# Optimization experiments

Measured on AMD Instinct MI355X. Metric: run time of the kernel, lower is better.

## Reference

```python
import jax, jax.numpy as jnp
import numpy as np

S, B, D, N, DH = 2048, 2, 1024, 16, 64  # seq, batch, d_model, n_head, d_head
LN_EPS = 1e-5


def setup_inputs() -> dict:
    key = jax.random.key(0)
    ks = jax.random.split(key, 8)
    h = jax.random.normal(ks[0], (S, B, D), dtype=jnp.float32)
    Wq = jax.random.normal(ks[1], (D, N * DH), dtype=jnp.float32) * 0.02
    Wkv = jax.random.normal(ks[2], (D, 2 * N * DH), dtype=jnp.float32) * 0.02
    Wo = jax.random.normal(ks[3], (N * DH, D), dtype=jnp.float32) * 0.02
    ln_gamma = jnp.ones((D,), dtype=jnp.float32)
    ln_beta = jnp.zeros((D,), dtype=jnp.float32)
    # persistent compressive-memory state from a previous segment
    memory = jax.random.normal(ks[4], (B, N, DH, DH), dtype=jnp.float32)
    # normalization is a sum of (elu(k)+1) over ~S positions -> strictly positive, O(S)
    mem_norm = jax.random.uniform(ks[5], (B, 1, N, DH), dtype=jnp.float32) * S + 1.0
    gate_beta = jnp.ones((1,), dtype=jnp.float32) * 0.01  # beta_eps
    return {"h": h, "Wq": Wq, "Wkv": Wkv, "Wo": Wo, "ln_gamma": ln_gamma,
            "ln_beta": ln_beta, "memory": memory, "mem_norm": mem_norm,
            "gate_beta": gate_beta}


def reference(h, Wq, Wkv, Wo, ln_gamma, ln_beta, memory, mem_norm, gate_beta):
    scale = 1.0 / np.sqrt(DH).astype(np.float32)
    # projections (pre_lnorm=False, mems=None -> c == h)
    q = (h @ Wq).reshape(S, B, N, DH)
    k, v = jnp.split(h @ Wkv, 2, axis=-1)
    k = k.reshape(S, B, N, DH)
    v = v.reshape(S, B, N, DH)
    # local quadratic attention
    score = jnp.einsum('ibnd,jbnd->ijbn', q, k) * scale  # [S,S,B,N]
    prob = jax.nn.softmax(score, axis=1)
    attn_vec = jnp.einsum('ijbn,jbnd->ibnd', prob, v).reshape(S, B, N * DH)
    # memory retrieval (NOTE: source swaps K/V in the _update_memory call;
    # it is done under no_grad -> stop_gradient here)
    cached_Q = jax.nn.elu(q.swapaxes(0, 1)) + 1.0          # [B,S,N,DH]
    num = jnp.einsum('bsnk,bnkv->bsnv', cached_Q, memory)   # [B,S,N,DH]
    den = jnp.einsum('bsnk,bvnk->bsnv', cached_Q, mem_norm)  # [B,S,N,1]
    content_A = jax.lax.stop_gradient(num / den)            # [B,S,N,DH]
    # gated injection
    g = jax.nn.sigmoid(gate_beta)                           # [1]
    inj = g * content_A.swapaxes(0, 1).reshape(S, B, N * DH) + (1.0 - g) * attn_vec
    attn_out = inj @ Wo
    # post layernorm residual
    y = h + attn_out
    mu = jnp.mean(y, axis=-1, keepdims=True)
    var = jnp.mean((y - mu) ** 2, axis=-1, keepdims=True)
    return (y - mu) / jnp.sqrt(var + LN_EPS) * ln_gamma + ln_beta
```

## Files before the change

### kernel.cpp

```cpp
#include <hip/hip_runtime.h>


typedef unsigned short ushort_t;
typedef unsigned int uint32;

typedef __bf16 bf16x8 __attribute__((ext_vector_type(8)));
typedef float f32x4 __attribute__((ext_vector_type(4)));
typedef float f32x16 __attribute__((ext_vector_type(16)));
typedef unsigned short u16x8 __attribute__((ext_vector_type(8)));
typedef unsigned short u16x4 __attribute__((ext_vector_type(4)));
typedef unsigned int u32x4 __attribute__((ext_vector_type(4)));

typedef const __attribute__((address_space(1))) void gvoid_t;
typedef __attribute__((address_space(3))) void lvoid_t;

#define S_LEN 2048
#define BATCH 2
#define NHEAD 16

__device__ __forceinline__ ushort_t f2bf(float x) {
  union { float f; unsigned u; } c; c.f = x;
  unsigned r = (c.u + 0x7FFFu + ((c.u >> 16) & 1u)) >> 16;
  return (ushort_t)r;
}
__device__ __forceinline__ float bf2f(ushort_t v) {
  union { unsigned u; float f; } c; c.u = ((unsigned)v) << 16;
  return c.f;
}

__global__ __launch_bounds__(256) void k_cvt_h(const float* __restrict__ src,
                                               ushort_t* __restrict__ dst, int n4) {
  int idx = blockIdx.x * 256 + threadIdx.x;
  if (idx >= n4) return;
  float4 v = ((const float4*)src)[idx];
  u16x4 o; o[0] = f2bf(v.x); o[1] = f2bf(v.y); o[2] = f2bf(v.z); o[3] = f2bf(v.w);
  ((u16x4*)dst)[idx] = o;
}

__global__ __launch_bounds__(256) void k_cvt_wT3(const float* __restrict__ Wq,
                                                 const float* __restrict__ Wkv,
                                                 const float* __restrict__ Wo,
                                                 ushort_t* __restrict__ wT,
                                                 ushort_t* __restrict__ woT) {
  const int z = blockIdx.z;
  const float* W;
  ushort_t* WT;
  int N;
  if (z == 0)      { W = Wq;  WT = wT;                          N = 1024; }
  else if (z == 1) { W = Wkv; WT = wT + (size_t)1024 * 1024;    N = 2048; }
  else             { W = Wo;  WT = woT;                         N = 1024; }
  const int K = 1024;
  if (blockIdx.x * 32 >= N) return;
  __shared__ float tile[32][33];
  const int n0 = blockIdx.x * 32, k0 = blockIdx.y * 32;
  const int tx = threadIdx.x & 31, ty = threadIdx.x >> 5;
#pragma unroll
  for (int r = 0; r < 32; r += 8)
    tile[ty + r][tx] = W[(size_t)(k0 + ty + r) * N + n0 + tx];
  __syncthreads();
#pragma unroll
  for (int r = 0; r < 32; r += 8)
    WT[(size_t)(n0 + ty + r) * K + k0 + tx] = f2bf(tile[tx][ty + r]);
}

template <int OUT_BF16>
__global__ __launch_bounds__(256) void k_gemm_bt(const ushort_t* __restrict__ A,
                                                 const ushort_t* __restrict__ B,
                                                 void* __restrict__ Cv, int M, int N, int K,
                                                 int nbx) {
  __shared__ __attribute__((aligned(16))) ushort_t As[128 * 64];
  __shared__ __attribute__((aligned(16))) ushort_t Bs[128 * 64];
  const int per = gridDim.x >> 3;
  const int fl = (blockIdx.x & 7) * per + (blockIdx.x >> 3);
  const int m0 = (fl / nbx) * 128, n0 = (fl % nbx) * 128;
  const int tid = threadIdx.x, w = tid >> 6, lane = tid & 63;
  const int wm = (w >> 1) * 64, wn = (w & 1) * 64;
  const int l15 = lane & 15, l4 = lane >> 4;
  const int sw = ((lane & 7) ^ (lane >> 3)) << 3;
  f32x4 acc[4][4];
#pragma unroll
  for (int i = 0; i < 4; ++i)
#pragma unroll
    for (int j = 0; j < 4; ++j)
#pragma unroll
      for (int r = 0; r < 4; ++r) acc[i][j][r] = 0.f;

  for (int k0 = 0; k0 < K; k0 += 64) {
    __syncthreads();
#pragma unroll
    for (int r = 0; r < 4; ++r) {
      int rowb = r * 32 + w * 8;
      const ushort_t* ga = A + (size_t)(m0 + rowb + (lane >> 3)) * K + k0 + sw;
      const ushort_t* gb = B + (size_t)(n0 + rowb + (lane >> 3)) * K + k0 + sw;
      __builtin_amdgcn_global_load_lds((gvoid_t*)ga, (lvoid_t*)(As + rowb * 64), 16, 0, 0);
      __builtin_amdgcn_global_load_lds((gvoid_t*)gb, (lvoid_t*)(Bs + rowb * 64), 16, 0, 0);
    }
    __syncthreads();
#pragma unroll
    for (int kk = 0; kk < 2; ++kk) {
      bf16x8 af[4], bfr[4];
#pragma unroll
      for (int i = 0; i < 4; ++i) {
        int row = wm + i * 16 + l15;
        af[i] = *(const bf16x8*)&As[row * 64 + (((kk * 4 + l4) ^ (row & 7)) << 3)];
      }
#pragma unroll
      for (int j = 0; j < 4; ++j) {
        int row = wn + j * 16 + l15;
        bfr[j] = *(const bf16x8*)&Bs[row * 64 + (((kk * 4 + l4) ^ (row & 7)) << 3)];
      }
#pragma unroll
      for (int i = 0; i < 4; ++i)
#pragma unroll
        for (int j = 0; j < 4; ++j)
          acc[i][j] = __builtin_amdgcn_mfma_f32_16x16x32_bf16(af[i], bfr[j], acc[i][j], 0, 0, 0);
    }
  }
#pragma unroll
  for (int i = 0; i < 4; ++i)
#pragma unroll
    for (int j = 0; j < 4; ++j)
#pragma unroll
      for (int r = 0; r < 4; ++r) {
        int row = m0 + wm + i * 16 + l4 * 4 + r;
        int col = n0 + wn + j * 16 + l15;
        if (OUT_BF16)
          ((ushort_t*)Cv)[(size_t)row * N + col] = f2bf(acc[i][j][r]);
        else
          ((float*)Cv)[(size_t)row * N + col] = acc[i][j][r];
      }
}

__global__ __launch_bounds__(256) void k_gemm64(const ushort_t* __restrict__ A,
                                                const ushort_t* __restrict__ B,
                                                float* __restrict__ C, int M, int N, int K,
                                                int nbx) {
  __shared__ __attribute__((aligned(16))) ushort_t As[64 * 32];
  __shared__ __attribute__((aligned(16))) ushort_t Bs[128 * 32];
  const int per = gridDim.x >> 3;
  const int fl = (blockIdx.x & 7) * per + (blockIdx.x >> 3);
  const int m0 = (fl / nbx) * 64, n0 = (fl % nbx) * 128;
  const int tid = threadIdx.x, w = tid >> 6, lane = tid & 63;
  const int wn = w * 32;
  const int l15 = lane & 15, l4 = lane >> 4;
  f32x4 acc[4][2];
#pragma unroll
  for (int i = 0; i < 4; ++i)
#pragma unroll
    for (int j = 0; j < 2; ++j)
#pragma unroll
      for (int r = 0; r < 4; ++r) acc[i][j][r] = 0.f;

  for (int k0 = 0; k0 < K; k0 += 32) {
    __syncthreads();
    {
      int c = w * 64 + lane;
      const ushort_t* ga = A + (size_t)(m0 + (c >> 2)) * K + k0 + (c & 3) * 8;
      __builtin_amdgcn_global_load_lds((gvoid_t*)ga, (lvoid_t*)(As + w * 512), 16, 0, 0);
#pragma unroll
      for (int r = 0; r < 2; ++r) {
        int c2 = r * 256 + w * 64 + lane;
        const ushort_t* gb = B + (size_t)(n0 + (c2 >> 2)) * K + k0 + (c2 & 3) * 8;
        __builtin_amdgcn_global_load_lds((gvoid_t*)gb, (lvoid_t*)(Bs + r * 2048 + w * 512), 16, 0, 0);
      }
    }
    __syncthreads();
    bf16x8 af[4], bfr[2];
#pragma unroll
    for (int i = 0; i < 4; ++i) af[i] = *(const bf16x8*)&As[(i * 16 + l15) * 32 + l4 * 8];
#pragma unroll
    for (int j = 0; j < 2; ++j) bfr[j] = *(const bf16x8*)&Bs[(wn + j * 16 + l15) * 32 + l4 * 8];
#pragma unroll
    for (int i = 0; i < 4; ++i)
#pragma unroll
      for (int j = 0; j < 2; ++j)
        acc[i][j] = __builtin_amdgcn_mfma_f32_16x16x32_bf16(af[i], bfr[j], acc[i][j], 0, 0, 0);
  }
#pragma unroll
  for (int i = 0; i < 4; ++i)
#pragma unroll
    for (int j = 0; j < 2; ++j)
#pragma unroll
      for (int r = 0; r < 4; ++r)
        C[(size_t)(m0 + i * 16 + l4 * 4 + r) * N + n0 + wn + j * 16 + l15] = acc[i][j][r];
}

__global__ __launch_bounds__(256) void k_vt(const ushort_t* __restrict__ qkv,
                                            ushort_t* __restrict__ vt) {
  __shared__ uint32 tile[64 * 65];
  const int jt = blockIdx.x, bn = blockIdx.y, b = bn & 1, n = bn >> 1;
  const int tid = threadIdx.x;
  const int j0 = jt * 64;
#pragma unroll
  for (int rr = 0; rr < 2; ++rr) {
    int lin = rr * 2048 + tid * 8;
    int j = lin >> 6, d0 = lin & 63;
    u16x8 v = *(const u16x8*)(qkv + (size_t)(j0 + j) * 6144 + b * 3072 + 2048 + n * 64 + d0);
#pragma unroll
    for (int e = 0; e < 8; ++e) tile[j * 65 + d0 + e] = v[e];
  }
  __syncthreads();
#pragma unroll
  for (int rr = 0; rr < 2; ++rr) {
    int lin = rr * 2048 + tid * 8;
    int d = lin >> 6, jj = lin & 63;
    u16x8 o;
#pragma unroll
    for (int e = 0; e < 8; ++e) o[e] = (ushort_t)tile[(jj + e) * 65 + d];
    *(u16x8*)(vt + ((size_t)bn * 64 + d) * 2048 + j0 + jj) = o;
  }
}

__global__ __launch_bounds__(256, 4) void k_attn(const ushort_t* __restrict__ qkv,
                                                 const ushort_t* __restrict__ vt,
                                                 ushort_t* o0, ushort_t* o1,
                                                 float* __restrict__ l0,
                                                 float* __restrict__ l1) {
  __shared__ __attribute__((aligned(16))) ushort_t Ks[2][4096];
  __shared__ __attribute__((aligned(16))) ushort_t VTs[2][4096];
  const int bn = blockIdx.y, b = bn & 1, n = bn >> 1, z = blockIdx.z;
  const int tid = threadIdx.x, w = tid >> 6, lane = tid & 63;
  const int l31 = lane & 31, h = lane >> 5;
  const int qrow = blockIdx.x * 128 + w * 32 + l31;
  const size_t qoff = (size_t)qrow * 6144 + b * 3072 + n * 64;
  const float CEXP = 0.18033688011113723f;
  bf16x8 qf[4];
#pragma unroll
  for (int ks = 0; ks < 4; ++ks) {
    u16x8 qv = *(const u16x8*)(qkv + qoff + ks * 16 + h * 8);
    union { u16x8 u; bf16x8 v; } cu;
#pragma unroll
    for (int e = 0; e < 8; ++e) cu.u[e] = f2bf(bf2f(qv[e]) * CEXP);
    qf[ks] = cu.v;
  }
  const int fA = (l31 & 7) ^ (l31 >> 3);
  const int fB = fA ^ 4;

  const int t0 = z * 16;
  const int sw0 = (((lane & 7) ^ (lane >> 3) ^ (w * 2)) & 7) << 3;
  const int sw1 = (((lane & 7) ^ (lane >> 3) ^ (w * 2 + 1)) & 7) << 3;
  const ushort_t* kp0 = qkv + (size_t)(t0 * 64 + w * 16 + (lane >> 3)) * 6144 + b * 3072 + n * 64 + 1024 + sw0;
  const ushort_t* kp1 = qkv + (size_t)(t0 * 64 + w * 16 + 8 + (lane >> 3)) * 6144 + b * 3072 + n * 64 + 1024 + sw1;
  const ushort_t* vp0 = vt + ((size_t)bn * 64 + w * 16 + (lane >> 3)) * 2048 + t0 * 64 + sw0;
  const ushort_t* vp1 = vt + ((size_t)bn * 64 + w * 16 + 8 + (lane >> 3)) * 2048 + t0 * 64 + sw1;
  const size_t KSTRIDE = (size_t)64 * 6144;

  __builtin_amdgcn_global_load_lds((gvoid_t*)kp0, (lvoid_t*)(Ks[0] + (w * 16) * 64), 16, 0, 0);
  __builtin_amdgcn_global_load_lds((gvoid_t*)kp1, (lvoid_t*)(Ks[0] + (w * 16 + 8) * 64), 16, 0, 0);
  __builtin_amdgcn_global_load_lds((gvoid_t*)vp0, (lvoid_t*)(VTs[0] + (w * 16) * 64), 16, 0, 0);
  __builtin_amdgcn_global_load_lds((gvoid_t*)vp1, (lvoid_t*)(VTs[0] + (w * 16 + 8) * 64), 16, 0, 0);
  kp0 += KSTRIDE; kp1 += KSTRIDE; vp0 += 64; vp1 += 64;
  __syncthreads();

  f32x16 oacc[2];
#pragma unroll
  for (int r = 0; r < 16; ++r) { oacc[0][r] = 0.f; oacc[1][r] = 0.f; }
  float lsum = 0.f;

  for (int t = 0; t < 16; ++t) {
    const ushort_t* Kb = Ks[t & 1];
    const ushort_t* Vb = VTs[t & 1];
    if (t < 15) {
      ushort_t* kw = Ks[(t + 1) & 1];
      ushort_t* vw = VTs[(t + 1) & 1];
      __builtin_amdgcn_global_load_lds((gvoid_t*)kp0, (lvoid_t*)(kw + (w * 16) * 64), 16, 0, 0);
      __builtin_amdgcn_global_load_lds((gvoid_t*)kp1, (lvoid_t*)(kw + (w * 16 + 8) * 64), 16, 0, 0);
      __builtin_amdgcn_global_load_lds((gvoid_t*)vp0, (lvoid_t*)(vw + (w * 16) * 64), 16, 0, 0);
      __builtin_amdgcn_global_load_lds((gvoid_t*)vp1, (lvoid_t*)(vw + (w * 16 + 8) * 64), 16, 0, 0);
      kp0 += KSTRIDE; kp1 += KSTRIDE; vp0 += 64; vp1 += 64;
    }
#pragma unroll
    for (int jb = 0; jb < 2; ++jb) {
      f32x16 sv;
#pragma unroll
      for (int r = 0; r < 16; ++r) sv[r] = 0.f;
      const int rb = (jb * 32 + l31) * 64;
      const int fj = jb ? fB : fA;
      __builtin_amdgcn_s_setprio(1);
#pragma unroll
      for (int ks = 0; ks < 4; ++ks) {
        bf16x8 kf = *(const bf16x8*)&Kb[rb + ((((ks << 1) | h) ^ fj) << 3)];
        sv = __builtin_amdgcn_mfma_f32_32x32x16_bf16(kf, qf[ks], sv, 0, 0, 0);
      }
      __builtin_amdgcn_s_setprio(0);
#pragma unroll
      for (int r = 0; r < 16; ++r) sv[r] = __builtin_amdgcn_exp2f(sv[r]);
#pragma unroll
      for (int ks2 = 0; ks2 < 2; ++ks2) {
        const int q0 = ks2 * 2;
        uint32 X0, X1, Y0, Y1;
        asm volatile("v_cvt_pk_bf16_f32 %0, %1, %2" : "=v"(X0) : "v"(sv[q0 * 4 + 0]), "v"(sv[q0 * 4 + 1]));
        asm volatile("v_cvt_pk_bf16_f32 %0, %1, %2" : "=v"(X1) : "v"(sv[q0 * 4 + 2]), "v"(sv[q0 * 4 + 3]));
        asm volatile("v_cvt_pk_bf16_f32 %0, %1, %2" : "=v"(Y0) : "v"(sv[(q0 + 1) * 4 + 0]), "v"(sv[(q0 + 1) * 4 + 1]));
        asm volatile("v_cvt_pk_bf16_f32 %0, %1, %2" : "=v"(Y1) : "v"(sv[(q0 + 1) * 4 + 2]), "v"(sv[(q0 + 1) * 4 + 3]));
        asm volatile("v_permlane32_swap_b32 %0, %1" : "+v"(X0), "+v"(Y0));
        asm volatile("v_permlane32_swap_b32 %0, %1" : "+v"(X1), "+v"(Y1));
        union { u32x4 u; bf16x8 v; } pf;
        pf.u[0] = X0; pf.u[1] = X1; pf.u[2] = Y0; pf.u[3] = Y1;
        const int c = ((jb * 2 + ks2) << 1) | h;
        bf16x8 vf0 = *(const bf16x8*)&Vb[l31 * 64 + ((c ^ fA) << 3)];
        bf16x8 vf1 = *(const bf16x8*)&Vb[(32 + l31) * 64 + ((c ^ fB) << 3)];
        __builtin_amdgcn_s_setprio(1);
        oacc[0] = __builtin_amdgcn_mfma_f32_32x32x16_bf16(vf0, pf.v, oacc[0], 0, 0, 0);
        oacc[1] = __builtin_amdgcn_mfma_f32_32x32x16_bf16(vf1, pf.v, oacc[1], 0, 0, 0);
        __builtin_amdgcn_s_setprio(0);
      }
      float ls[8];
#pragma unroll
      for (int r = 0; r < 8; ++r) ls[r] = sv[r] + sv[r + 8];
#pragma unroll
      for (int st = 4; st >= 1; st >>= 1)
#pragma unroll
        for (int r = 0; r < st; ++r) ls[r] += ls[r + st];
      lsum += ls[0];
    }
    if (t < 15) __syncthreads();
  }
  const float l_run = lsum + __shfl_xor(lsum, 32);

  ushort_t* op = (z == 0) ? (o0 + (size_t)qrow * 2048 + b * 1024 + n * 64)
                          : (o1 + (size_t)qrow * 6144 + b * 3072 + 2048 + n * 64);
#pragma unroll
  for (int db = 0; db < 2; ++db)
#pragma unroll
    for (int qq = 0; qq < 4; ++qq) {
      u16x4 st;
#pragma unroll
      for (int m = 0; m < 4; ++m) st[m] = f2bf(oacc[db][qq * 4 + m]);
      *(u16x4*)(op + db * 32 + qq * 8 + h * 4) = st;
    }
  if (h == 0) {
    float* lp = (z == 0) ? l0 : l1;
    lp[qrow * 32 + bn] = l_run;
  }
}

__global__ __launch_bounds__(256) void k_gate2(const ushort_t* __restrict__ qkv,
                                               const ushort_t* __restrict__ o0,
                                               const float* __restrict__ l0,
                                               const float* __restrict__ l1,
                                               const float* __restrict__ mem,
                                               const float* __restrict__ mnorm,
                                               const float* __restrict__ gbeta,
                                               ushort_t* __restrict__ inj) {
  const int bn = blockIdx.y, b = bn & 1, n = bn >> 1;
  const int tid = threadIdx.x, w = tid >> 6, lane = tid & 63;
  const int l31 = lane & 31, h = lane >> 5;
  const int qrow = blockIdx.x * 128 + w * 32 + l31;
  const size_t qoff = (size_t)qrow * 6144 + b * 3072 + n * 64;

  float den = 0.f;
  bf16x8 cqf[4];
  const float* nrm = mnorm + (size_t)(b * NHEAD + n) * 64;
#pragma unroll
  for (int ks = 0; ks < 4; ++ks) {
    u16x8 qv = *(const u16x8*)(qkv + qoff + ks * 16 + h * 8);
    union { u16x8 u; bf16x8 v; } cu;
#pragma unroll
    for (int e = 0; e < 8; ++e) {
      float x = bf2f(qv[e]);
      float c = (x > 0.f) ? (x + 1.f) : __builtin_amdgcn_exp2f(x * 1.4426950408889634f);
      cu.u[e] = f2bf(c);
      den += c * nrm[ks * 16 + h * 8 + e];
    }
    cqf[ks] = cu.v;
  }
  den += __shfl_xor(den, 32);

  const float* mb = mem + (size_t)(b * NHEAD + n) * 4096;
  f32x16 accv[2];
#pragma unroll
  for (int r = 0; r < 16; ++r) { accv[0][r] = 0.f; accv[1][r] = 0.f; }
#pragma unroll
  for (int db = 0; db < 2; ++db)
#pragma unroll
    for (int ks = 0; ks < 4; ++ks) {
      union { u16x8 u; bf16x8 v; } af;
#pragma unroll
      for (int e = 0; e < 8; ++e)
        af.u[e] = f2bf(mb[(size_t)(ks * 16 + h * 8 + e) * 64 + db * 32 + l31]);
      accv[db] = __builtin_amdgcn_mfma_f32_32x32x16_bf16(af.v, cqf[ks], accv[db], 0, 0, 0);
    }

  const float lsum = l0[qrow * 32 + bn] + l1[qrow * 32 + bn];
  float g = 1.f / (1.f + expf(-gbeta[0]));
  float rden = 1.f / den, invl = 1.f / lsum;
  const ushort_t* p0 = o0 + (size_t)qrow * 2048 + b * 1024 + n * 64;
  const ushort_t* p1 = qkv + (size_t)qrow * 6144 + b * 3072 + 2048 + n * 64;
  ushort_t* op = inj + (size_t)qrow * 2048 + b * 1024 + n * 64;
#pragma unroll
  for (int db = 0; db < 2; ++db)
#pragma unroll
    for (int qq = 0; qq < 4; ++qq) {
      const int off = db * 32 + qq * 8 + h * 4;
      u16x4 a0 = *(const u16x4*)(p0 + off);
      u16x4 a1 = *(const u16x4*)(p1 + off);
      u16x4 st;
#pragma unroll
      for (int m = 0; m < 4; ++m) {
        float av = (bf2f(a0[m]) + bf2f(a1[m])) * invl;
        float content = accv[db][qq * 4 + m] * rden;
        st[m] = f2bf(g * content + (1.f - g) * av);
      }
      *(u16x4*)(op + off) = st;
    }
}

__global__ __launch_bounds__(256) void k_ln(const float* __restrict__ h,
                                            const float* __restrict__ ao,
                                            const float* __restrict__ gam,
                                            const float* __restrict__ bet,
                                            float* __restrict__ out) {
  const int m = blockIdx.x, t = threadIdx.x;
  const int lane = t & 63, w = t >> 6;
  __shared__ float redS[4], redQ[4];
  const size_t base = (size_t)m * 1024;
  float4 hv = ((const float4*)(h + base))[t];
  float4 avv = ((const float4*)(ao + base))[t];
  float y0 = hv.x + avv.x, y1 = hv.y + avv.y, y2 = hv.z + avv.z, y3 = hv.w + avv.w;
  float s = y0 + y1 + y2 + y3;
  float sq = y0 * y0 + y1 * y1 + y2 * y2 + y3 * y3;
#pragma unroll
  for (int mk = 32; mk >= 1; mk >>= 1) { s += __shfl_xor(s, mk); sq += __shfl_xor(sq, mk); }
  if (lane == 0) { redS[w] = s; redQ[w] = sq; }
  __syncthreads();
  float Ssum = redS[0] + redS[1] + redS[2] + redS[3];
  float Qsum = redQ[0] + redQ[1] + redQ[2] + redQ[3];
  float mu = Ssum * (1.f / 1024.f);
  float var = Qsum * (1.f / 1024.f) - mu * mu;
  float rstd = rsqrtf(var + 1e-5f);
  float4 g = ((const float4*)gam)[t];
  float4 bt = ((const float4*)bet)[t];
  float4 o;
  o.x = (y0 - mu) * rstd * g.x + bt.x;
  o.y = (y1 - mu) * rstd * g.y + bt.y;
  o.z = (y2 - mu) * rstd * g.z + bt.z;
  o.w = (y3 - mu) * rstd * g.w + bt.w;
  ((float4*)(out + base))[t] = o;
}

extern "C" void kernel_launch(void* const* d_in, const int* in_sizes, int n_in,
                              void* d_out, int out_size, void* d_ws, size_t ws_size,
                              hipStream_t stream) {
  const float* h = (const float*)d_in[0];
  const float* Wq = (const float*)d_in[1];
  const float* Wkv = (const float*)d_in[2];
  const float* Wo = (const float*)d_in[3];
  const float* gam = (const float*)d_in[4];
  const float* bet = (const float*)d_in[5];
  const float* mem = (const float*)d_in[6];
  const float* mnorm = (const float*)d_in[7];
  const float* gbeta = (const float*)d_in[8];
  float* out = (float*)d_out;

  char* ws = (char*)d_ws;
  ushort_t* hb  = (ushort_t*)(ws);
  ushort_t* wT  = (ushort_t*)(ws + (size_t)(8u << 20));
  ushort_t* woT = (ushort_t*)(ws + (size_t)(14u << 20));
  ushort_t* qkv = (ushort_t*)(ws + (size_t)(16u << 20));
  float*    ao  = (float*)   (ws + (size_t)(16u << 20));
  ushort_t* vtb = (ushort_t*)(ws + (size_t)(40u << 20));
  ushort_t* o0  = hb;
  float*    l0  = (float*)(ws + (size_t)(8u << 20));
  float*    l1  = (float*)(ws + (size_t)(8u << 20) + (1u << 18));
  ushort_t* inj = vtb;

  k_cvt_h<<<4096, 256, 0, stream>>>(h, hb, 1048576);
  k_cvt_wT3<<<dim3(64, 32, 3), 256, 0, stream>>>(Wq, Wkv, Wo, wT, woT);
  k_gemm_bt<1><<<768, 256, 0, stream>>>(hb, wT, (void*)qkv, 4096, 3072, 1024, 24);
  k_vt<<<dim3(32, 32), 256, 0, stream>>>(qkv, vtb);
  k_attn<<<dim3(16, 32, 2), 256, 0, stream>>>(qkv, vtb, o0, qkv, l0, l1);
  k_gate2<<<dim3(16, 32), 256, 0, stream>>>(qkv, o0, l0, l1, mem, mnorm, gbeta, inj);
  k_gemm64<<<512, 256, 0, stream>>>(inj, woT, ao, 4096, 1024, 1024, 8);
  k_ln<<<4096, 256, 0, stream>>>(h, ao, gam, bet, out);
}
```

Measured before the change: 144.4 us.

## Merge conversion kernels and deepen output GEMM K-tile with swizzled LDS

The separate h-to-bf16 and weight-transpose kernels become one launch, with an extra z-slice that converts h. The output-projection GEMM now loads 64-wide K tiles instead of 32, halving loop iterations and barriers. It also uses an XOR swizzle on LDS addresses to avoid bank conflicts on the fragment reads. LDS use per block doubles, which may lower occupancy.

```diff
diff --git a/kernel.cpp b/kernel.cpp
--- a/kernel.cpp
+++ b/kernel.cpp
@@ -28,27 +28,31 @@
   return c.f;
 }
 
-__global__ __launch_bounds__(256) void k_cvt_h(const float* __restrict__ src,
-                                               ushort_t* __restrict__ dst, int n4) {
-  int idx = blockIdx.x * 256 + threadIdx.x;
-  if (idx >= n4) return;
-  float4 v = ((const float4*)src)[idx];
-  u16x4 o; o[0] = f2bf(v.x); o[1] = f2bf(v.y); o[2] = f2bf(v.z); o[3] = f2bf(v.w);
-  ((u16x4*)dst)[idx] = o;
-}
-
-__global__ __launch_bounds__(256) void k_cvt_wT3(const float* __restrict__ Wq,
+__global__ __launch_bounds__(256) void k_cvt_all(const float* __restrict__ h,
+                                                 const float* __restrict__ Wq,
                                                  const float* __restrict__ Wkv,
                                                  const float* __restrict__ Wo,
+                                                 ushort_t* __restrict__ hb,
                                                  ushort_t* __restrict__ wT,
                                                  ushort_t* __restrict__ woT) {
   const int z = blockIdx.z;
+  if (z == 3) {
+    int idx = (blockIdx.y * 64 + blockIdx.x) * 256 + threadIdx.x;
+#pragma unroll
+    for (int i = 0; i < 2; ++i) {
+      int e = idx + i * 524288;
+      float4 v = ((const float4*)h)[e];
+      u16x4 o; o[0] = f2bf(v.x); o[1] = f2bf(v.y); o[2] = f2bf(v.z); o[3] = f2bf(v.w);
+      ((u16x4*)hb)[e] = o;
+    }
+    return;
+  }
   const float* W;
   ushort_t* WT;
   int N;
-  if (z == 0)      { W = Wq;  WT = wT;                          N = 1024; }
-  else if (z == 1) { W = Wkv; WT = wT + (size_t)1024 * 1024;    N = 2048; }
-  else             { W = Wo;  WT = woT;                         N = 1024; }
+  if (z == 0)      { W = Wq;  WT = wT;                        N = 1024; }
+  else if (z == 1) { W = Wkv; WT = wT + (size_t)1024 * 1024;  N = 2048; }
+  else             { W = Wo;  WT = woT;                       N = 1024; }
   const int K = 1024;
   if (blockIdx.x * 32 >= N) return;
   __shared__ float tile[32][33];
@@ -135,14 +139,15 @@
                                                 const ushort_t* __restrict__ B,
                                                 float* __restrict__ C, int M, int N, int K,
                                                 int nbx) {
-  __shared__ __attribute__((aligned(16))) ushort_t As[64 * 32];
-  __shared__ __attribute__((aligned(16))) ushort_t Bs[128 * 32];
+  __shared__ __attribute__((aligned(16))) ushort_t As[64 * 64];
+  __shared__ __attribute__((aligned(16))) ushort_t Bs[128 * 64];
   const int per = gridDim.x >> 3;
   const int fl = (blockIdx.x & 7) * per + (blockIdx.x >> 3);
   const int m0 = (fl / nbx) * 64, n0 = (fl % nbx) * 128;
   const int tid = threadIdx.x, w = tid >> 6, lane = tid & 63;
   const int wn = w * 32;
   const int l15 = lane & 15, l4 = lane >> 4;
+  const int sw = ((lane & 7) ^ (lane >> 3)) << 3;
   f32x4 acc[4][2];
 #pragma unroll
   for (int i = 0; i < 4; ++i)
@@ -151,30 +156,40 @@
 #pragma unroll
       for (int r = 0; r < 4; ++r) acc[i][j][r] = 0.f;
 
-  for (int k0 = 0; k0 < K; k0 += 32) {
+  for (int k0 = 0; k0 < K; k0 += 64) {
     __syncthreads();
-    {
-      int c = w * 64 + lane;
-      const ushort_t* ga = A + (size_t)(m0 + (c >> 2)) * K + k0 + (c & 3) * 8;
-      __builtin_amdgcn_global_load_lds((gvoid_t*)ga, (lvoid_t*)(As + w * 512), 16, 0, 0);
-#pragma unroll
-      for (int r = 0; r < 2; ++r) {
-        int c2 = r * 256 + w * 64 + lane;
-        const ushort_t* gb = B + (size_t)(n0 + (c2 >> 2)) * K + k0 + (c2 & 3) * 8;
-        __builtin_amdgcn_global_load_lds((gvoid_t*)gb, (lvoid_t*)(Bs + r * 2048 + w * 512), 16, 0, 0);
-      }
+#pragma unroll
+    for (int r = 0; r < 2; ++r) {
+      int rowb = w * 16 + r * 8;
+      const ushort_t* ga = A + (size_t)(m0 + rowb + (lane >> 3)) * K + k0 + sw;
+      __builtin_amdgcn_global_load_lds((gvoid_t*)ga, (lvoid_t*)(As + rowb * 64), 16, 0, 0);
+    }
+#pragma unroll
+    for (int r = 0; r < 4; ++r) {
+      int rowb = w * 32 + r * 8;
+      const ushort_t* gb = B + (size_t)(n0 + rowb + (lane >> 3)) * K + k0 + sw;
+      __builtin_amdgcn_global_load_lds((gvoid_t*)gb, (lvoid_t*)(Bs + rowb * 64), 16, 0, 0);
     }
     __syncthreads();
-    bf16x8 af[4], bfr[2];
-#pragma unroll
-    for (int i = 0; i < 4; ++i) af[i] = *(const bf16x8*)&As[(i * 16 + l15) * 32 + l4 * 8];
-#pragma unroll
-    for (int j = 0; j < 2; ++j) bfr[j] = *(const bf16x8*)&Bs[(wn + j * 16 + l15) * 32 + l4 * 8];
-#pragma unroll
-    for (int i = 0; i < 4; ++i)
-#pragma unroll
-      for (int j = 0; j < 2; ++j)
-        acc[i][j] = __builtin_amdgcn_mfma_f32_16x16x32_bf16(af[i], bfr[j], acc[i][j], 0, 0, 0);
+#pragma unroll
+    for (int kk = 0; kk < 2; ++kk) {
+      bf16x8 af[4], bfr[2];
+#pragma unroll
+      for (int i = 0; i < 4; ++i) {
+        int row = i * 16 + l15;
+        af[i] = *(const bf16x8*)&As[row * 64 + (((kk * 4 + l4) ^ (row & 7)) << 3)];
+      }
+#pragma unroll
+      for (int j = 0; j < 2; ++j) {
+        int row = wn + j * 16 + l15;
+        bfr[j] = *(const bf16x8*)&Bs[row * 64 + (((kk * 4 + l4) ^ (row & 7)) << 3)];
+      }
+#pragma unroll
+      for (int i = 0; i < 4; ++i)
+#pragma unroll
+        for (int j = 0; j < 2; ++j)
+          acc[i][j] = __builtin_amdgcn_mfma_f32_16x16x32_bf16(af[i], bfr[j], acc[i][j], 0, 0, 0);
+    }
   }
 #pragma unroll
   for (int i = 0; i < 4; ++i)
@@ -465,8 +480,7 @@
   float*    l1  = (float*)(ws + (size_t)(8u << 20) + (1u << 18));
   ushort_t* inj = vtb;
 
-  k_cvt_h<<<4096, 256, 0, stream>>>(h, hb, 1048576);
-  k_cvt_wT3<<<dim3(64, 32, 3), 256, 0, stream>>>(Wq, Wkv, Wo, wT, woT);
+  k_cvt_all<<<dim3(64, 32, 4), 256, 0, stream>>>(h, Wq, Wkv, Wo, hb, wT, woT);
   k_gemm_bt<1><<<768, 256, 0, stream>>>(hb, wT, (void*)qkv, 4096, 3072, 1024, 24);
   k_vt<<<dim3(32, 32), 256, 0, stream>>>(qkv, vtb);
   k_attn<<<dim3(16, 32, 2), 256, 0, stream>>>(qkv, vtb, o0, qkv, l0, l1);
```

New measurement: 138.3 us. 1.04x faster.
